# Kernel tuning notes

Hardware: AMD Instinct MI355X
Metric: run time of the kernel (lower is better)

## Reference

```python
import jax, jax.numpy as jnp
import numpy as np

VOCAB = 4194304
EMBED = 128
BATCH = 16384
NUM_DENSE = 13
NUM_CAT = 26
BOT_DIMS = (512, 256, 128)
TOP_DIMS = (1024, 1024, 512, 256, 1)


def _dense_params(key, fan_in, fan_out):
    kw, kb = jax.random.split(key)
    w = jax.random.normal(kw, (fan_in, fan_out), jnp.float32) * np.sqrt(2.0 / (fan_in + fan_out))
    b = jax.random.normal(kb, (fan_out,), jnp.float32) * np.sqrt(1.0 / fan_out)
    return w, b


def setup_inputs() -> dict:
    key = jax.random.key(0)
    ks = jax.random.split(key, 16)
    inp = {}
    inp['x_dense'] = jax.random.normal(ks[0], (BATCH, NUM_DENSE), jnp.float32)
    inp['x_cat'] = jax.random.randint(ks[1], (BATCH, NUM_CAT), 0, VOCAB, dtype=jnp.int32)
    # embedding table: uniform(0,1) * 1/sqrt(vocab)
    inp['embedding_table'] = jax.random.uniform(ks[2], (VOCAB, EMBED), jnp.float32) * np.float32(1.0 / np.sqrt(VOCAB))
    # bottom MLP params
    fan_in = NUM_DENSE
    for i, d in enumerate(BOT_DIMS):
        w, b = _dense_params(ks[3 + i], fan_in, d)
        inp[f'w_bot{i}'], inp[f'b_bot{i}'] = w, b
        fan_in = d
    # top MLP params; input dim = embed_dim + n_triu(27) = 128 + 378 = 506
    n_feat = 1 + NUM_CAT  # 27
    fan_in = EMBED + n_feat * (n_feat + 1) // 2
    for i, d in enumerate(TOP_DIMS):
        w, b = _dense_params(ks[8 + i], fan_in, d)
        inp[f'w_top{i}'], inp[f'b_top{i}'] = w, b
        fan_in = d
    return inp


def _forward(x_dense, x_cat, embedding_table,
             w_bot0, b_bot0, w_bot1, b_bot1, w_bot2, b_bot2,
             w_top0, b_top0, w_top1, b_top1, w_top2, b_top2,
             w_top3, b_top3, w_top4, b_top4):
    B = x_dense.shape[0]
    # bottom MLP
    h = x_dense
    for w, b in ((w_bot0, b_bot0), (w_bot1, b_bot1), (w_bot2, b_bot2)):
        h = jax.nn.relu(h @ w + b)
    bot_out = h  # [B, 128]
    feat = bot_out.reshape(B, -1, EMBED)  # [B, 1, 128]
    # embedding gather (irregular access)
    idx = (x_cat.reshape(-1) % VOCAB)
    emb = embedding_table[idx].reshape(B, NUM_CAT, EMBED)  # [B, 26, 128]
    stack = jnp.concatenate([feat, emb], axis=1)  # [B, 27, 128]
    # self interaction + upper-triangular (incl. diagonal) extraction
    xact = jnp.einsum('bnd,bmd->bnm', stack, stack)  # [B, 27, 27]
    i, j = jnp.triu_indices(stack.shape[1])
    inter = xact[:, i, j]  # [B, 378]
    top = jnp.concatenate([bot_out, inter], axis=-1)  # [B, 506]
    tops = ((w_top0, b_top0), (w_top1, b_top1), (w_top2, b_top2), (w_top3, b_top3), (w_top4, b_top4))
    for li, (w, b) in enumerate(tops):
        top = top @ w + b
        if li < len(tops) - 1:
            top = jax.nn.relu(top)
    return top  # [B, 1] logits


def reference(x_dense, x_cat, embedding_table,
              w_bot0, b_bot0, w_bot1, b_bot1, w_bot2, b_bot2,
              w_top0, b_top0, w_top1, b_top1, w_top2, b_top2,
              w_top3, b_top3, w_top4, b_top4):
    return _forward(x_dense, x_cat, embedding_table,
                    w_bot0, b_bot0, w_bot1, b_bot1, w_bot2, b_bot2,
                    w_top0, b_top0, w_top1, b_top1, w_top2, b_top2,
                    w_top3, b_top3, w_top4, b_top4)
```

## Files before the change

kernel.cpp:

```cpp
#include <hip/hip_runtime.h>
#include <cstdint>
#include <cstddef>

#define BATCH 16384
#define VOCAB_MASK (4194304 - 1)

typedef __attribute__((ext_vector_type(4))) float f32x4;
typedef __attribute__((ext_vector_type(8))) __bf16 bf16x8;
typedef __attribute__((ext_vector_type(4))) __bf16 bf16x4;

static_assert(sizeof(bf16x8) == 16, "bf16x8 must be 16 bytes");

static __device__ __forceinline__ __bf16 f2bf(float f) {
  union { float f; unsigned u; } in; in.f = f;
  unsigned r = in.u + 0x7FFF + ((in.u >> 16) & 1);
  union { unsigned short s; __bf16 b; } out; out.s = (unsigned short)(r >> 16);
  return out.b;
}
static __device__ __forceinline__ float bf2f(__bf16 b) {
  union { __bf16 b; unsigned short s; } in; in.b = b;
  union { unsigned u; float f; } out; out.u = ((unsigned)in.s) << 16;
  return out.f;
}

#define GLDS16(g, l) __builtin_amdgcn_global_load_lds( \
    (const __attribute__((address_space(1))) unsigned int*)(g), \
    (__attribute__((address_space(3))) unsigned int*)(l), 16, 0, 0)

static __device__ __forceinline__ unsigned swz16(unsigned b) {
  return b ^ ((((b >> 6) & 3u) ^ ((b >> 8) & 3u)) << 4);
}
static __device__ __forceinline__ bf16x8 lds_frag(const char* smem, unsigned base,
                                                  unsigned r, unsigned cg) {
  unsigned b = r * 64u + cg;
  return *(const bf16x8*)(smem + base + swz16(b));
}

struct TJob { const float* W; __bf16* WT; int K, N, Kp, tx, off; };
struct TJobs { TJob j[7]; };

__global__ __launch_bounds__(256) void transpose_all(TJobs js, int njobs)
{
  __shared__ float tile[64][65];
  int b = blockIdx.x;
  int ji = 0;
  #pragma unroll
  for (int i = 1; i < 7; ++i) if (i < njobs && b >= js.j[i].off) ji = i;
  const TJob jb = js.j[ji];
  int lb = b - jb.off;
  int bx = lb % jb.tx, by = lb / jb.tx;
  const int kb = bx * 64, nb = by * 64;
  const int tx = threadIdx.x & 63, ty = threadIdx.x >> 6;
  #pragma unroll
  for (int i = 0; i < 64; i += 4) {
    int k = kb + ty + i, n = nb + tx;
    tile[ty + i][tx] = (k < jb.K && n < jb.N) ? jb.W[(size_t)k * jb.N + n] : 0.f;
  }
  __syncthreads();
  #pragma unroll
  for (int i = 0; i < 64; i += 4) {
    int n = nb + ty + i, k = kb + tx;
    if (n < jb.N && k < jb.Kp) jb.WT[(size_t)n * jb.Kp + k] = f2bf(tile[tx][ty + i]);
  }
}

__global__ __launch_bounds__(256) void bottom_fused(
    const float* __restrict__ x,
    const __bf16* __restrict__ w0t, const float* __restrict__ b0,
    const __bf16* __restrict__ w1t, const float* __restrict__ b1,
    const __bf16* __restrict__ w2t, const float* __restrict__ b2,
    __bf16* __restrict__ h2out)
{
  __shared__ __bf16 h0s[32][520];
  __shared__ __bf16 h1s[32][264];
  __shared__ __bf16 As[32][40];
  __shared__ __bf16 Bs[256][32];
  const int tid = threadIdx.x, lane = tid & 63, w = tid >> 6;
  const int r0 = blockIdx.x * 32;
  const int srow_b = lane >> 2;
  const int scol_b = (lane & 3) * 8;
  const unsigned rA = lane & 15, cgw = (lane >> 4) * 8;

  for (int idx = tid; idx < 32 * 40; idx += 256) {
    int row = idx / 40, k = idx - row * 40;
    float v = (k < 13) ? x[(size_t)(r0 + row) * 13 + k] : 0.f;
    As[row][k] = f2bf(v);
  }

  #pragma unroll
  for (int p = 0; p < 2; ++p) {
    __syncthreads();
    #pragma unroll
    for (int c = 0; c < 4; ++c) {
      int row = w * 64 + c * 16 + srow_b;
      GLDS16(w0t + (size_t)(p * 256 + row) * 32 + scol_b, &Bs[row][scol_b]);
    }
    __syncthreads();
    bf16x8 a[2], bv[4];
    #pragma unroll
    for (int m = 0; m < 2; ++m) a[m] = *(const bf16x8*)&As[rA + m * 16][cgw];
    #pragma unroll
    for (int n = 0; n < 4; ++n) bv[n] = *(const bf16x8*)&Bs[w * 64 + n * 16 + rA][cgw];
    f32x4 acc[2][4] = {};
    #pragma unroll
    for (int m = 0; m < 2; ++m)
      #pragma unroll
      for (int n = 0; n < 4; ++n)
        acc[m][n] = __builtin_amdgcn_mfma_f32_16x16x32_bf16(a[m], bv[n], acc[m][n], 0, 0, 0);
    #pragma unroll
    for (int m = 0; m < 2; ++m)
      #pragma unroll
      for (int n = 0; n < 4; ++n) {
        int col = p * 256 + w * 64 + n * 16 + (int)rA;
        float bb = b0[col];
        #pragma unroll
        for (int r = 0; r < 4; ++r) {
          int row = m * 16 + (lane >> 4) * 4 + r;
          h0s[row][col] = f2bf(fmaxf(acc[m][n][r] + bb, 0.f));
        }
      }
  }

  f32x4 acc1[2][4] = {};
  for (int k0 = 0; k0 < 512; k0 += 32) {
    __syncthreads();
    #pragma unroll
    for (int c = 0; c < 4; ++c) {
      int row = w * 64 + c * 16 + srow_b;
      GLDS16(w1t + (size_t)row * 512 + k0 + scol_b, &Bs[row][scol_b]);
    }
    __syncthreads();
    bf16x8 a[2], bv[4];
    #pragma unroll
    for (int m = 0; m < 2; ++m) a[m] = *(const bf16x8*)&h0s[rA + m * 16][k0 + cgw];
    #pragma unroll
    for (int n = 0; n < 4; ++n) bv[n] = *(const bf16x8*)&Bs[w * 64 + n * 16 + rA][cgw];
    #pragma unroll
    for (int m = 0; m < 2; ++m)
      #pragma unroll
      for (int n = 0; n < 4; ++n)
        acc1[m][n] = __builtin_amdgcn_mfma_f32_16x16x32_bf16(a[m], bv[n], acc1[m][n], 0, 0, 0);
  }
  #pragma unroll
  for (int m = 0; m < 2; ++m)
    #pragma unroll
    for (int n = 0; n < 4; ++n) {
      int col = w * 64 + n * 16 + (int)rA;
      float bb = b1[col];
      #pragma unroll
      for (int r = 0; r < 4; ++r) {
        int row = m * 16 + (lane >> 4) * 4 + r;
        h1s[row][col] = f2bf(fmaxf(acc1[m][n][r] + bb, 0.f));
      }
    }

  f32x4 acc2[2][2] = {};
  for (int k0 = 0; k0 < 256; k0 += 32) {
    __syncthreads();
    #pragma unroll
    for (int c = 0; c < 2; ++c) {
      int row = w * 32 + c * 16 + srow_b;
      GLDS16(w2t + (size_t)row * 256 + k0 + scol_b, &Bs[row][scol_b]);
    }
    __syncthreads();
    bf16x8 a[2], bv[2];
    #pragma unroll
    for (int m = 0; m < 2; ++m) a[m] = *(const bf16x8*)&h1s[rA + m * 16][k0 + cgw];
    #pragma unroll
    for (int n = 0; n < 2; ++n) bv[n] = *(const bf16x8*)&Bs[w * 32 + n * 16 + rA][cgw];
    #pragma unroll
    for (int m = 0; m < 2; ++m)
      #pragma unroll
      for (int n = 0; n < 2; ++n)
        acc2[m][n] = __builtin_amdgcn_mfma_f32_16x16x32_bf16(a[m], bv[n], acc2[m][n], 0, 0, 0);
  }
  #pragma unroll
  for (int m = 0; m < 2; ++m)
    #pragma unroll
    for (int n = 0; n < 2; ++n) {
      int col = w * 32 + n * 16 + (int)rA;
      float bb = b2[col];
      #pragma unroll
      for (int r = 0; r < 4; ++r) {
        int row = m * 16 + (lane >> 4) * 4 + r;
        h2out[(size_t)(r0 + row) * 128 + col] = f2bf(fmaxf(acc2[m][n][r] + bb, 0.f));
      }
    }
}

__global__ __launch_bounds__(256) void interact_mfma(
    const __bf16* __restrict__ bot, const int* __restrict__ xcat,
    const float* __restrict__ emb, __bf16* __restrict__ top_in)
{
  __shared__ __bf16 st[4][32][136];
  const int tid = threadIdx.x, lane = tid & 63, w = tid >> 6;
  const int s = blockIdx.x * 4 + w;

  const int* xr = xcat + (size_t)s * 26;
  float4 buf[13];
  #pragma unroll
  for (int i = 0; i < 13; ++i) {
    int fi = 2 * i + (lane >> 5);
    int ridx = xr[fi] & VOCAB_MASK;
    buf[i] = *(const float4*)(emb + (size_t)ridx * 128 + (lane & 31) * 4);
  }

  *(unsigned*)&st[w][0][lane * 2] = *(const unsigned*)(bot + (size_t)s * 128 + lane * 2);
  #pragma unroll
  for (int r = 27; r < 32; ++r) *(unsigned*)&st[w][r][lane * 2] = 0u;
  #pragma unroll
  for (int i = 0; i < 13; ++i) {
    int row = 1 + 2 * i + (lane >> 5);
    bf16x4 bv;
    bv[0] = f2bf(buf[i].x); bv[1] = f2bf(buf[i].y);
    bv[2] = f2bf(buf[i].z); bv[3] = f2bf(buf[i].w);
    *(bf16x4*)&st[w][row][(lane & 31) * 4] = bv;
  }

  f32x4 a00 = {}, a01 = {}, a11 = {};
  #pragma unroll
  for (int k0 = 0; k0 < 4; ++k0) {
    bf16x8 fr0 = *(const bf16x8*)&st[w][(lane & 15)][k0 * 32 + (lane >> 4) * 8];
    bf16x8 fr1 = *(const bf16x8*)&st[w][16 + (lane & 15)][k0 * 32 + (lane >> 4) * 8];
    a00 = __builtin_amdgcn_mfma_f32_16x16x32_bf16(fr0, fr0, a00, 0, 0, 0);
    a01 = __builtin_amdgcn_mfma_f32_16x16x32_bf16(fr0, fr1, a01, 0, 0, 0);
    a11 = __builtin_amdgcn_mfma_f32_16x16x32_bf16(fr1, fr1, a11, 0, 0, 0);
  }

  __bf16* op = top_in + (size_t)s * 512;
  ((unsigned*)op)[lane] = *(const unsigned*)&st[w][0][lane * 2];
  if (lane < 3) ((unsigned*)op)[253 + lane] = 0u;

  const int jc = lane & 15, rb = (lane >> 4) * 4;
  #pragma unroll
  for (int r = 0; r < 4; ++r) {
    {
      int i = rb + r, j = jc;
      if (i <= j) op[128 + i * 27 - i * (i - 1) / 2 + (j - i)] = f2bf(a00[r]);
    }
    {
      int i = rb + r, j = 16 + jc;
      if (j <= 26) op[128 + i * 27 - i * (i - 1) / 2 + (j - i)] = f2bf(a01[r]);
    }
    {
      int i = 16 + rb + r, j = 16 + jc;
      if (i <= j && j <= 26) op[128 + i * 27 - i * (i - 1) / 2 + (j - i)] = f2bf(a11[r]);
    }
  }
}

__global__ __launch_bounds__(512, 4) void gemm_8ph_bm128(
    const __bf16* __restrict__ A, const __bf16* __restrict__ WT,
    const float* __restrict__ bias, __bf16* __restrict__ C,
    int N, int sA, int K, int gm)
{
  __shared__ __align__(16) char smem[49152];
  const int tid = threadIdx.x, lane = tid & 63, w = tid >> 6;
  const int wm = w >> 2, wn = w & 3;

  int nb = gridDim.x;
  int id = blockIdx.x;
  int swz = ((nb & 7) == 0) ? ((id & 7) * (nb >> 3) + (id >> 3)) : id;
  const int m0 = (swz % gm) * 128, n0 = (swz / gm) * 256;

  unsigned LdA; const __bf16* sApA;
  {
    unsigned L = (unsigned)w * 1024u + (unsigned)lane * 16u;
    unsigned Ls = swz16(L);
    LdA = L;
    sApA = A + (size_t)(m0 + (Ls >> 6)) * sA + ((Ls & 63) >> 1);
  }
  unsigned LdB[2]; const __bf16* sBp[2];
  #pragma unroll
  for (int h = 0; h < 2; ++h) {
    unsigned L = h * 8192u + (unsigned)w * 1024u + (unsigned)lane * 16u;
    unsigned Ls = swz16(L);
    LdB[h] = L;
    sBp[h] = WT + (size_t)(n0 + (Ls >> 6)) * K + ((Ls & 63) >> 1);
  }

  #define STAGE_A1(kt, p) { GLDS16(sApA + (kt)*32, smem + (p)*24576 + LdA); }
  #define STAGE_B2(kt, p) { GLDS16(sBp[0] + (kt)*32, smem + (p)*24576 + 8192 + LdB[0]); \
                            GLDS16(sBp[1] + (kt)*32, smem + (p)*24576 + 8192 + LdB[1]); }

  const unsigned cg = (lane >> 4) * 16u;
  const unsigned rA = (lane & 15);

  f32x4 acc[4][4] = {};
  const int iters = (K >> 5) >> 1;

  STAGE_B2(0, 0); STAGE_A1(0, 0); STAGE_B2(1, 1);
  asm volatile("s_waitcnt vmcnt(2)" ::: "memory");
  __builtin_amdgcn_s_barrier();
  __builtin_amdgcn_sched_barrier(0);

  for (int i = 0; i < iters; ++i) {
    const int t = 2 * i;
    const bool more = (i + 1 < iters);

    bf16x8 a0[2], b0[4];
    #pragma unroll
    for (int m = 0; m < 2; ++m) a0[m] = lds_frag(smem, 0, wm * 64 + m * 16 + rA, cg);
    #pragma unroll
    for (int n = 0; n < 4; ++n) b0[n] = lds_frag(smem, 8192, wn * 64 + n * 16 + rA, cg);
    STAGE_A1(t + 1, 1);
    __builtin_amdgcn_s_barrier();
    asm volatile("s_waitcnt lgkmcnt(0)" ::: "memory");
    __builtin_amdgcn_sched_barrier(0);
    __builtin_amdgcn_s_setprio(1);
    #pragma unroll
    for (int m = 0; m < 2; ++m)
      #pragma unroll
      for (int n = 0; n < 4; ++n)
        acc[m][n] = __builtin_amdgcn_mfma_f32_16x16x32_bf16(a0[m], b0[n], acc[m][n], 0, 0, 0);
    __builtin_amdgcn_s_setprio(0);
    __builtin_amdgcn_s_barrier();
    __builtin_amdgcn_sched_barrier(0);

    bf16x8 a1[2];
    #pragma unroll
    for (int m = 0; m < 2; ++m) a1[m] = lds_frag(smem, 0, wm * 64 + 32 + m * 16 + rA, cg);
    if (more) STAGE_B2(t + 2, 0);
    __builtin_amdgcn_s_barrier();
    asm volatile("s_waitcnt lgkmcnt(0)" ::: "memory");
    __builtin_amdgcn_sched_barrier(0);
    __builtin_amdgcn_s_setprio(1);
    #pragma unroll
    for (int m = 0; m < 2; ++m)
      #pragma unroll
      for (int n = 0; n < 4; ++n)
        acc[2 + m][n] = __builtin_amdgcn_mfma_f32_16x16x32_bf16(a1[m], b0[n], acc[2 + m][n], 0, 0, 0);
    __builtin_amdgcn_s_setprio(0);
    if (more) { asm volatile("s_waitcnt vmcnt(2)" ::: "memory"); }
    else      { asm volatile("s_waitcnt vmcnt(0)" ::: "memory"); }
    __builtin_amdgcn_s_barrier();
    __builtin_amdgcn_sched_barrier(0);

    bf16x8 a2[2], b2[4];
    #pragma unroll
    for (int m = 0; m < 2; ++m) a2[m] = lds_frag(smem, 24576, wm * 64 + m * 16 + rA, cg);
    #pragma unroll
    for (int n = 0; n < 4; ++n) b2[n] = lds_frag(smem, 24576 + 8192, wn * 64 + n * 16 + rA, cg);
    if (more) STAGE_A1(t + 2, 0);
    __builtin_amdgcn_s_barrier();
    asm volatile("s_waitcnt lgkmcnt(0)" ::: "memory");
    __builtin_amdgcn_sched_barrier(0);
    __builtin_amdgcn_s_setprio(1);
    #pragma unroll
    for (int m = 0; m < 2; ++m)
      #pragma unroll
      for (int n = 0; n < 4; ++n)
        acc[m][n] = __builtin_amdgcn_mfma_f32_16x16x32_bf16(a2[m], b2[n], acc[m][n], 0, 0, 0);
    __builtin_amdgcn_s_setprio(0);
    __builtin_amdgcn_s_barrier();
    __builtin_amdgcn_sched_barrier(0);

    bf16x8 a3[2];
    #pragma unroll
    for (int m = 0; m < 2; ++m) a3[m] = lds_frag(smem, 24576, wm * 64 + 32 + m * 16 + rA, cg);
    if (more) STAGE_B2(t + 3, 1);
    __builtin_amdgcn_s_barrier();
    asm volatile("s_waitcnt lgkmcnt(0)" ::: "memory");
    __builtin_amdgcn_sched_barrier(0);
    __builtin_amdgcn_s_setprio(1);
    #pragma unroll
    for (int m = 0; m < 2; ++m)
      #pragma unroll
      for (int n = 0; n < 4; ++n)
        acc[2 + m][n] = __builtin_amdgcn_mfma_f32_16x16x32_bf16(a3[m], b2[n], acc[2 + m][n], 0, 0, 0);
    __builtin_amdgcn_s_setprio(0);
    if (more) { asm volatile("s_waitcnt vmcnt(2)" ::: "memory"); }
    __builtin_amdgcn_s_barrier();
    __builtin_amdgcn_sched_barrier(0);
  }

  #pragma unroll
  for (int n = 0; n < 4; ++n) {
    int col = n0 + wn * 64 + n * 16 + (lane & 15);
    float bv = bias[col];
    #pragma unroll
    for (int m = 0; m < 4; ++m) {
      #pragma unroll
      for (int r = 0; r < 4; ++r) {
        int row = m0 + wm * 64 + m * 16 + (lane >> 4) * 4 + r;
        float v = fmaxf(acc[m][n][r] + bv, 0.f);
        C[(size_t)row * N + col] = f2bf(v);
      }
    }
  }
  #undef STAGE_A1
  #undef STAGE_B2
}

__global__ __launch_bounds__(512, 2) void gemm_8ph_n128(
    const __bf16* __restrict__ A, const __bf16* __restrict__ WT,
    const float* __restrict__ bias, __bf16* __restrict__ C,
    int N, int sA, int K, int gm)
{
  __shared__ __align__(16) char smem[49152];
  const int tid = threadIdx.x, lane = tid & 63, w = tid >> 6;
  const int wm = w >> 1, wn = w & 1;

  int nb = gridDim.x;
  int id = blockIdx.x;
  int swz = ((nb & 7) == 0) ? ((id & 7) * (nb >> 3) + (id >> 3)) : id;
  const int m0 = (swz % gm) * 256, n0 = (swz / gm) * 128;

  unsigned Ld[2]; const __bf16* sAp[2]; const __bf16* sBp0;
  #pragma unroll
  for (int h = 0; h < 2; ++h) {
    unsigned L = h * 8192u + (unsigned)w * 1024u + (unsigned)lane * 16u;
    unsigned Ls = swz16(L);
    Ld[h] = L;
    int srow = Ls >> 6, scb = Ls & 63;
    sAp[h] = A + (size_t)(m0 + srow) * sA + (scb >> 1);
  }
  {
    unsigned L = (unsigned)w * 1024u + (unsigned)lane * 16u;
    unsigned Ls = swz16(L);
    int srow = Ls >> 6, scb = Ls & 63;
    sBp0 = WT + (size_t)(n0 + srow) * K + (scb >> 1);
  }

  #define STAGE_A2(kt, p) { GLDS16(sAp[0] + (kt)*32, smem + (p)*24576 + Ld[0]); \
                            GLDS16(sAp[1] + (kt)*32, smem + (p)*24576 + Ld[1]); }
  #define STAGE_B1(kt, p) { GLDS16(sBp0 + (kt)*32, smem + (p)*24576 + 16384 + Ld[0]); }

  const unsigned cg = (lane >> 4) * 16u;
  const unsigned rA = (lane & 15);

  f32x4 acc[4][4] = {};
  const int iters = (K >> 5) >> 1;

  STAGE_B1(0, 0); STAGE_A2(0, 0); STAGE_B1(1, 1);
  asm volatile("s_waitcnt vmcnt(1)" ::: "memory");
  __builtin_amdgcn_s_barrier();
  __builtin_amdgcn_sched_barrier(0);

  for (int i = 0; i < iters; ++i) {
    const int t = 2 * i;
    const bool more = (i + 1 < iters);

    bf16x8 a0[2], b0[4];
    #pragma unroll
    for (int m = 0; m < 2; ++m) a0[m] = lds_frag(smem, 0, wm * 64 + m * 16 + rA, cg);
    #pragma unroll
    for (int n = 0; n < 4; ++n) b0[n] = lds_frag(smem, 16384, wn * 64 + n * 16 + rA, cg);
    STAGE_A2(t + 1, 1);
    __builtin_amdgcn_s_barrier();
    asm volatile("s_waitcnt lgkmcnt(0)" ::: "memory");
    __builtin_amdgcn_sched_barrier(0);
    __builtin_amdgcn_s_setprio(1);
    #pragma unroll
    for (int m = 0; m < 2; ++m)
      #pragma unroll
      for (int n = 0; n < 4; ++n)
        acc[m][n] = __builtin_amdgcn_mfma_f32_16x16x32_bf16(a0[m], b0[n], acc[m][n], 0, 0, 0);
    __builtin_amdgcn_s_setprio(0);
    __builtin_amdgcn_s_barrier();
    __builtin_amdgcn_sched_barrier(0);

    bf16x8 a1[2];
    #pragma unroll
    for (int m = 0; m < 2; ++m) a1[m] = lds_frag(smem, 0, wm * 64 + 32 + m * 16 + rA, cg);
    if (more) STAGE_B1(t + 2, 0);
    __builtin_amdgcn_s_barrier();
    asm volatile("s_waitcnt lgkmcnt(0)" ::: "memory");
    __builtin_amdgcn_sched_barrier(0);
    __builtin_amdgcn_s_setprio(1);
    #pragma unroll
    for (int m = 0; m < 2; ++m)
      #pragma unroll
      for (int n = 0; n < 4; ++n)
        acc[2 + m][n] = __builtin_amdgcn_mfma_f32_16x16x32_bf16(a1[m], b0[n], acc[2 + m][n], 0, 0, 0);
    __builtin_amdgcn_s_setprio(0);
    if (more) { asm volatile("s_waitcnt vmcnt(1)" ::: "memory"); }
    else      { asm volatile("s_waitcnt vmcnt(0)" ::: "memory"); }
    __builtin_amdgcn_s_barrier();
    __builtin_amdgcn_sched_barrier(0);

    bf16x8 a2[2], b2[4];
    #pragma unroll
    for (int m = 0; m < 2; ++m) a2[m] = lds_frag(smem, 24576, wm * 64 + m * 16 + rA, cg);
    #pragma unroll
    for (int n = 0; n < 4; ++n) b2[n] = lds_frag(smem, 24576 + 16384, wn * 64 + n * 16 + rA, cg);
    if (more) STAGE_A2(t + 2, 0);
    __builtin_amdgcn_s_barrier();
    asm volatile("s_waitcnt lgkmcnt(0)" ::: "memory");
    __builtin_amdgcn_sched_barrier(0);
    __builtin_amdgcn_s_setprio(1);
    #pragma unroll
    for (int m = 0; m < 2; ++m)
      #pragma unroll
      for (int n = 0; n < 4; ++n)
        acc[m][n] = __builtin_amdgcn_mfma_f32_16x16x32_bf16(a2[m], b2[n], acc[m][n], 0, 0, 0);
    __builtin_amdgcn_s_setprio(0);
    __builtin_amdgcn_s_barrier();
    __builtin_amdgcn_sched_barrier(0);

    bf16x8 a3[2];
    #pragma unroll
    for (int m = 0; m < 2; ++m) a3[m] = lds_frag(smem, 24576, wm * 64 + 32 + m * 16 + rA, cg);
    if (more) STAGE_B1(t + 3, 1);
    __builtin_amdgcn_s_barrier();
    asm volatile("s_waitcnt lgkmcnt(0)" ::: "memory");
    __builtin_amdgcn_sched_barrier(0);
    __builtin_amdgcn_s_setprio(1);
    #pragma unroll
    for (int m = 0; m < 2; ++m)
      #pragma unroll
      for (int n = 0; n < 4; ++n)
        acc[2 + m][n] = __builtin_amdgcn_mfma_f32_16x16x32_bf16(a3[m], b2[n], acc[2 + m][n], 0, 0, 0);
    __builtin_amdgcn_s_setprio(0);
    if (more) { asm volatile("s_waitcnt vmcnt(1)" ::: "memory"); }
    __builtin_amdgcn_s_barrier();
    __builtin_amdgcn_sched_barrier(0);
  }

  #pragma unroll
  for (int n = 0; n < 4; ++n) {
    int col = n0 + wn * 64 + n * 16 + (lane & 15);
    float bv = bias[col];
    #pragma unroll
    for (int m = 0; m < 4; ++m) {
      #pragma unroll
      for (int r = 0; r < 4; ++r) {
        int row = m0 + wm * 64 + m * 16 + (lane >> 4) * 4 + r;
        float v = fmaxf(acc[m][n][r] + bv, 0.f);
        C[(size_t)row * N + col] = f2bf(v);
      }
    }
  }
  #undef STAGE_A2
  #undef STAGE_B1
}

__global__ __launch_bounds__(256) void gemm_t3_final(
    const __bf16* __restrict__ A, const __bf16* __restrict__ WT,
    const float* __restrict__ b3, const float* __restrict__ w4,
    const float* __restrict__ b4, float* __restrict__ out)
{
  __shared__ __bf16 As[128][32];
  __shared__ __bf16 Bs[256][32];
  __shared__ float red[128][4];
  const int tid = threadIdx.x, lane = tid & 63, wid = tid >> 6;
  const int m0 = blockIdx.x * 128;
  const int srow = wid * 16 + (lane >> 2);
  const int scol = (lane & 3) * 8;
  const __bf16* Ag0 = A + (size_t)(m0 + srow) * 512 + scol;
  const __bf16* Ag1 = A + (size_t)(m0 + srow + 64) * 512 + scol;

  f32x4 acc[8][4] = {};

  for (int k0 = 0; k0 < 512; k0 += 32) {
    __syncthreads();
    GLDS16(Ag0 + k0, &As[srow][scol]);
    GLDS16(Ag1 + k0, &As[srow + 64][scol]);
    #pragma unroll
    for (int c = 0; c < 4; ++c) {
      int br = wid * 64 + c * 16 + (lane >> 2);
      GLDS16(WT + (size_t)br * 512 + k0 + scol, &Bs[br][scol]);
    }
    __syncthreads();

    bf16x8 af[8], bfv[4];
    #pragma unroll
    for (int m = 0; m < 8; ++m)
      af[m] = *(const bf16x8*)&As[m * 16 + (lane & 15)][(lane >> 4) * 8];
    #pragma unroll
    for (int n = 0; n < 4; ++n)
      bfv[n] = *(const bf16x8*)&Bs[wid * 64 + n * 16 + (lane & 15)][(lane >> 4) * 8];
    #pragma unroll
    for (int m = 0; m < 8; ++m)
      #pragma unroll
      for (int n = 0; n < 4; ++n)
        acc[m][n] = __builtin_amdgcn_mfma_f32_16x16x32_bf16(af[m], bfv[n], acc[m][n], 0, 0, 0);
  }

  float pd[8][4];
  #pragma unroll
  for (int m = 0; m < 8; ++m)
    #pragma unroll
    for (int r = 0; r < 4; ++r) pd[m][r] = 0.f;
  #pragma unroll
  for (int n = 0; n < 4; ++n) {
    int col = wid * 64 + n * 16 + (lane & 15);
    float bb = b3[col];
    float wc = w4[col];
    #pragma unroll
    for (int m = 0; m < 8; ++m)
      #pragma unroll
      for (int r = 0; r < 4; ++r)
        pd[m][r] += fmaxf(acc[m][n][r] + bb, 0.f) * wc;
  }
  #pragma unroll
  for (int m = 0; m < 8; ++m)
    #pragma unroll
    for (int r = 0; r < 4; ++r) {
      float s = pd[m][r];
      s += __shfl_xor(s, 1); s += __shfl_xor(s, 2);
      s += __shfl_xor(s, 4); s += __shfl_xor(s, 8);
      if ((lane & 15) == 0) red[m * 16 + (lane >> 4) * 4 + r][wid] = s;
    }
  __syncthreads();
  if (tid < 128)
    out[m0 + tid] = red[tid][0] + red[tid][1] + red[tid][2] + red[tid][3] + b4[0];
}

extern "C" void kernel_launch(void* const* d_in, const int* in_sizes, int n_in,
                              void* d_out, int out_size, void* d_ws, size_t ws_size,
                              hipStream_t stream)
{
  const float* x_dense = (const float*)d_in[0];
  const int*   x_cat   = (const int*)d_in[1];
  const float* emb     = (const float*)d_in[2];
  const float* wb[3] = {(const float*)d_in[3], (const float*)d_in[5], (const float*)d_in[7]};
  const float* bb[3] = {(const float*)d_in[4], (const float*)d_in[6], (const float*)d_in[8]};
  const float* wt[5] = {(const float*)d_in[9],  (const float*)d_in[11], (const float*)d_in[13],
                        (const float*)d_in[15], (const float*)d_in[17]};
  const float* bt[5] = {(const float*)d_in[10], (const float*)d_in[12], (const float*)d_in[14],
                        (const float*)d_in[16], (const float*)d_in[18]};
  float* out = (float*)d_out;

  char* ws = (char*)d_ws;
  const size_t MB = 1ull << 20;
  __bf16* wt_b0 = (__bf16*)(ws + 0 * MB);
  __bf16* wt_b1 = (__bf16*)(ws + 1 * MB);
  __bf16* wt_b2 = (__bf16*)(ws + 2 * MB);
  __bf16* wt_t0 = (__bf16*)(ws + 3 * MB);
  __bf16* wt_t1 = (__bf16*)(ws + 4 * MB);
  __bf16* wt_t2 = (__bf16*)(ws + 6 * MB);
  __bf16* wt_t3 = (__bf16*)(ws + 7 * MB);
  __bf16* h2     = (__bf16*)(ws + 8 * MB);
  __bf16* top_in = (__bf16*)(ws + 12 * MB);
  __bf16* t2     = (__bf16*)(ws + 12 * MB);
  __bf16* t1     = (__bf16*)(ws + 28 * MB);
  __bf16* t0     = (__bf16*)(ws + 60 * MB);

  TJobs js;
  const float* Ws[7] = {wb[0], wb[1], wb[2], wt[0], wt[1], wt[2], wt[3]};
  __bf16* WTs[7] = {wt_b0, wt_b1, wt_b2, wt_t0, wt_t1, wt_t2, wt_t3};
  int Ks[7]  = {13, 512, 256, 506, 1024, 1024, 512};
  int Ns[7]  = {512, 256, 128, 1024, 1024, 512, 256};
  int Kps[7] = {32, 512, 256, 512, 1024, 1024, 512};
  int off = 0;
  for (int i = 0; i < 7; ++i) {
    int tx = (Kps[i] + 63) / 64, ty = (Ns[i] + 63) / 64;
    js.j[i] = TJob{Ws[i], WTs[i], Ks[i], Ns[i], Kps[i], tx, off};
    off += tx * ty;
  }
  transpose_all<<<dim3(off), dim3(256), 0, stream>>>(js, 7);

  bottom_fused<<<dim3(BATCH / 32), dim3(256), 0, stream>>>(
      x_dense, wt_b0, bb[0], wt_b1, bb[1], wt_b2, bb[2], h2);

  interact_mfma<<<dim3(BATCH / 4), dim3(256), 0, stream>>>(h2, x_cat, emb, top_in);

  gemm_8ph_bm128<<<dim3(512), dim3(512), 0, stream>>>(top_in, wt_t0, bt[0], t0, 1024, 512, 512, 128);
  gemm_8ph_bm128<<<dim3(512), dim3(512), 0, stream>>>(t0, wt_t1, bt[1], t1, 1024, 1024, 1024, 128);
  gemm_8ph_n128<<<dim3(256), dim3(512), 0, stream>>>(t1, wt_t2, bt[2], t2, 512, 1024, 1024, 64);

  gemm_t3_final<<<dim3(128), dim3(256), 0, stream>>>(t2, wt_t3, bt[3], wt[4], bt[4], out);
}
```

Measured before the change: 189.2 us.

## Replace top-MLP GEMM with 256x256 tile, 4-stage LDS pipeline kernel

Swaps the 128x256-tile double-buffered GEMM for the first two top-MLP layers for a 256x256-tile kernel with a 4-deep LDS ring (128 KB shared) and three k-tiles of prefetch in flight. The larger tile doubles per-wave accumulators and raises MFMA work per LDS fragment load. The deeper pipeline aims to hide global-load latency better. In exchange, grid size halves to 256 blocks, occupancy drops with the large LDS and register footprint, and the wait counts must match the deeper prefetch.

Result: slower. 202.5 us (+7.0%).

```diff
diff --git a/kernel.cpp b/kernel.cpp
--- a/kernel.cpp
+++ b/kernel.cpp
@@ -249,147 +249,118 @@
   }
 }
 
-__global__ __launch_bounds__(512, 4) void gemm_8ph_bm128(
+__global__ __launch_bounds__(512, 2) void gemm_deep(
     const __bf16* __restrict__ A, const __bf16* __restrict__ WT,
     const float* __restrict__ bias, __bf16* __restrict__ C,
     int N, int sA, int K, int gm)
 {
-  __shared__ __align__(16) char smem[49152];
+  __shared__ __align__(16) char smem[131072];
   const int tid = threadIdx.x, lane = tid & 63, w = tid >> 6;
   const int wm = w >> 2, wn = w & 3;
 
   int nb = gridDim.x;
   int id = blockIdx.x;
   int swz = ((nb & 7) == 0) ? ((id & 7) * (nb >> 3) + (id >> 3)) : id;
-  const int m0 = (swz % gm) * 128, n0 = (swz / gm) * 256;
-
-  unsigned LdA; const __bf16* sApA;
-  {
-    unsigned L = (unsigned)w * 1024u + (unsigned)lane * 16u;
-    unsigned Ls = swz16(L);
-    LdA = L;
-    sApA = A + (size_t)(m0 + (Ls >> 6)) * sA + ((Ls & 63) >> 1);
-  }
-  unsigned LdB[2]; const __bf16* sBp[2];
+  const int m0 = (swz % gm) * 256, n0 = (swz / gm) * 256;
+
+  unsigned Ld[2]; const __bf16* sAp[2]; const __bf16* sBp[2];
   #pragma unroll
   for (int h = 0; h < 2; ++h) {
     unsigned L = h * 8192u + (unsigned)w * 1024u + (unsigned)lane * 16u;
     unsigned Ls = swz16(L);
-    LdB[h] = L;
-    sBp[h] = WT + (size_t)(n0 + (Ls >> 6)) * K + ((Ls & 63) >> 1);
-  }
-
-  #define STAGE_A1(kt, p) { GLDS16(sApA + (kt)*32, smem + (p)*24576 + LdA); }
-  #define STAGE_B2(kt, p) { GLDS16(sBp[0] + (kt)*32, smem + (p)*24576 + 8192 + LdB[0]); \
-                            GLDS16(sBp[1] + (kt)*32, smem + (p)*24576 + 8192 + LdB[1]); }
+    Ld[h] = L;
+    int srow = Ls >> 6, scb = Ls & 63;
+    sAp[h] = A  + (size_t)(m0 + srow) * sA + (scb >> 1);
+    sBp[h] = WT + (size_t)(n0 + srow) * K  + (scb >> 1);
+  }
+
+  #define STAGE_A(kt, p) { GLDS16(sAp[0] + (size_t)(kt)*32, smem + (p)*32768 + Ld[0]); \
+                           GLDS16(sAp[1] + (size_t)(kt)*32, smem + (p)*32768 + Ld[1]); }
+  #define STAGE_B(kt, p) { GLDS16(sBp[0] + (size_t)(kt)*32, smem + (p)*32768 + 16384 + Ld[0]); \
+                           GLDS16(sBp[1] + (size_t)(kt)*32, smem + (p)*32768 + 16384 + Ld[1]); }
 
   const unsigned cg = (lane >> 4) * 16u;
   const unsigned rA = (lane & 15);
 
-  f32x4 acc[4][4] = {};
-  const int iters = (K >> 5) >> 1;
-
-  STAGE_B2(0, 0); STAGE_A1(0, 0); STAGE_B2(1, 1);
-  asm volatile("s_waitcnt vmcnt(2)" ::: "memory");
+  f32x4 acc[8][4] = {};
+  const int KT = K >> 5;
+
+  STAGE_B(0, 0); STAGE_A(0, 0);
+  STAGE_B(1, 1); STAGE_A(1, 1);
+  STAGE_B(2, 2); STAGE_A(2, 2);
+  asm volatile("s_waitcnt vmcnt(8)" ::: "memory");
   __builtin_amdgcn_s_barrier();
   __builtin_amdgcn_sched_barrier(0);
 
-  for (int i = 0; i < iters; ++i) {
-    const int t = 2 * i;
-    const bool more = (i + 1 < iters);
-
-    bf16x8 a0[2], b0[4];
-    #pragma unroll
-    for (int m = 0; m < 2; ++m) a0[m] = lds_frag(smem, 0, wm * 64 + m * 16 + rA, cg);
-    #pragma unroll
-    for (int n = 0; n < 4; ++n) b0[n] = lds_frag(smem, 8192, wn * 64 + n * 16 + rA, cg);
-    STAGE_A1(t + 1, 1);
-    __builtin_amdgcn_s_barrier();
-    asm volatile("s_waitcnt lgkmcnt(0)" ::: "memory");
-    __builtin_amdgcn_sched_barrier(0);
-    __builtin_amdgcn_s_setprio(1);
-    #pragma unroll
-    for (int m = 0; m < 2; ++m)
-      #pragma unroll
-      for (int n = 0; n < 4; ++n)
-        acc[m][n] = __builtin_amdgcn_mfma_f32_16x16x32_bf16(a0[m], b0[n], acc[m][n], 0, 0, 0);
-    __builtin_amdgcn_s_setprio(0);
-    __builtin_amdgcn_s_barrier();
-    __builtin_amdgcn_sched_barrier(0);
-
-    bf16x8 a1[2];
-    #pragma unroll
-    for (int m = 0; m < 2; ++m) a1[m] = lds_frag(smem, 0, wm * 64 + 32 + m * 16 + rA, cg);
-    if (more) STAGE_B2(t + 2, 0);
-    __builtin_amdgcn_s_barrier();
-    asm volatile("s_waitcnt lgkmcnt(0)" ::: "memory");
-    __builtin_amdgcn_sched_barrier(0);
-    __builtin_amdgcn_s_setprio(1);
-    #pragma unroll
-    for (int m = 0; m < 2; ++m)
-      #pragma unroll
-      for (int n = 0; n < 4; ++n)
-        acc[2 + m][n] = __builtin_amdgcn_mfma_f32_16x16x32_bf16(a1[m], b0[n], acc[2 + m][n], 0, 0, 0);
-    __builtin_amdgcn_s_setprio(0);
-    if (more) { asm volatile("s_waitcnt vmcnt(2)" ::: "memory"); }
-    else      { asm volatile("s_waitcnt vmcnt(0)" ::: "memory"); }
-    __builtin_amdgcn_s_barrier();
-    __builtin_amdgcn_sched_barrier(0);
-
-    bf16x8 a2[2], b2[4];
-    #pragma unroll
-    for (int m = 0; m < 2; ++m) a2[m] = lds_frag(smem, 24576, wm * 64 + m * 16 + rA, cg);
-    #pragma unroll
-    for (int n = 0; n < 4; ++n) b2[n] = lds_frag(smem, 24576 + 8192, wn * 64 + n * 16 + rA, cg);
-    if (more) STAGE_A1(t + 2, 0);
-    __builtin_amdgcn_s_barrier();
-    asm volatile("s_waitcnt lgkmcnt(0)" ::: "memory");
-    __builtin_amdgcn_sched_barrier(0);
-    __builtin_amdgcn_s_setprio(1);
-    #pragma unroll
-    for (int m = 0; m < 2; ++m)
-      #pragma unroll
-      for (int n = 0; n < 4; ++n)
-        acc[m][n] = __builtin_amdgcn_mfma_f32_16x16x32_bf16(a2[m], b2[n], acc[m][n], 0, 0, 0);
-    __builtin_amdgcn_s_setprio(0);
-    __builtin_amdgcn_s_barrier();
-    __builtin_amdgcn_sched_barrier(0);
-
-    bf16x8 a3[2];
-    #pragma unroll
-    for (int m = 0; m < 2; ++m) a3[m] = lds_frag(smem, 24576, wm * 64 + 32 + m * 16 + rA, cg);
-    if (more) STAGE_B2(t + 3, 1);
-    __builtin_amdgcn_s_barrier();
-    asm volatile("s_waitcnt lgkmcnt(0)" ::: "memory");
-    __builtin_amdgcn_sched_barrier(0);
-    __builtin_amdgcn_s_setprio(1);
-    #pragma unroll
-    for (int m = 0; m < 2; ++m)
-      #pragma unroll
-      for (int n = 0; n < 4; ++n)
-        acc[2 + m][n] = __builtin_amdgcn_mfma_f32_16x16x32_bf16(a3[m], b2[n], acc[2 + m][n], 0, 0, 0);
-    __builtin_amdgcn_s_setprio(0);
-    if (more) { asm volatile("s_waitcnt vmcnt(2)" ::: "memory"); }
-    __builtin_amdgcn_s_barrier();
-    __builtin_amdgcn_sched_barrier(0);
-  }
+  #define TILE_BODY(j) { \
+    const int t = mi * 4 + (j); \
+    const bool stg = (t + 3 < KT); \
+     \
+    bf16x8 a0[4], b0[4]; \
+    _Pragma("unroll") \
+    for (int m = 0; m < 4; ++m) a0[m] = lds_frag(smem, (j)*32768u, wm * 128 + m * 16 + rA, cg); \
+    _Pragma("unroll") \
+    for (int n = 0; n < 4; ++n) b0[n] = lds_frag(smem, (j)*32768u + 16384u, wn * 64 + n * 16 + rA, cg); \
+    if (stg) STAGE_A(t + 3, ((j) + 3) & 3); \
+    __builtin_amdgcn_s_barrier(); \
+    asm volatile("s_waitcnt lgkmcnt(0)" ::: "memory"); \
+    __builtin_amdgcn_sched_barrier(0); \
+    __builtin_amdgcn_s_setprio(1); \
+    _Pragma("unroll") \
+    for (int m = 0; m < 4; ++m) \
+      _Pragma("unroll") \
+      for (int n = 0; n < 4; ++n) \
+        acc[m][n] = __builtin_amdgcn_mfma_f32_16x16x32_bf16(a0[m], b0[n], acc[m][n], 0, 0, 0); \
+    __builtin_amdgcn_s_setprio(0); \
+    __builtin_amdgcn_s_barrier(); \
+    __builtin_amdgcn_sched_barrier(0); \
+     \
+    bf16x8 a1[4]; \
+    _Pragma("unroll") \
+    for (int m = 0; m < 4; ++m) a1[m] = lds_frag(smem, (j)*32768u, wm * 128 + 64 + m * 16 + rA, cg); \
+    if (stg) STAGE_B(t + 3, ((j) + 3) & 3); \
+    __builtin_amdgcn_s_barrier(); \
+    asm volatile("s_waitcnt lgkmcnt(0)" ::: "memory"); \
+    __builtin_amdgcn_sched_barrier(0); \
+    __builtin_amdgcn_s_setprio(1); \
+    _Pragma("unroll") \
+    for (int m = 0; m < 4; ++m) \
+      _Pragma("unroll") \
+      for (int n = 0; n < 4; ++n) \
+        acc[4 + m][n] = __builtin_amdgcn_mfma_f32_16x16x32_bf16(a1[m], b0[n], acc[4 + m][n], 0, 0, 0); \
+    __builtin_amdgcn_s_setprio(0); \
+    if (t + 4 <= KT - 1)      { asm volatile("s_waitcnt vmcnt(8)" ::: "memory"); } \
+    else if (t + 3 == KT - 1) { asm volatile("s_waitcnt vmcnt(4)" ::: "memory"); } \
+    else                      { asm volatile("s_waitcnt vmcnt(0)" ::: "memory"); } \
+    __builtin_amdgcn_s_barrier(); \
+    __builtin_amdgcn_sched_barrier(0); \
+  }
+
+  const int MI = KT >> 2;
+  for (int mi = 0; mi < MI; ++mi) {
+    TILE_BODY(0)
+    TILE_BODY(1)
+    TILE_BODY(2)
+    TILE_BODY(3)
+  }
+  #undef TILE_BODY
+  #undef STAGE_A
+  #undef STAGE_B
 
   #pragma unroll
   for (int n = 0; n < 4; ++n) {
     int col = n0 + wn * 64 + n * 16 + (lane & 15);
     float bv = bias[col];
     #pragma unroll
-    for (int m = 0; m < 4; ++m) {
+    for (int m = 0; m < 8; ++m) {
       #pragma unroll
       for (int r = 0; r < 4; ++r) {
-        int row = m0 + wm * 64 + m * 16 + (lane >> 4) * 4 + r;
+        int row = m0 + wm * 128 + m * 16 + (lane >> 4) * 4 + r;
         float v = fmaxf(acc[m][n][r] + bv, 0.f);
         C[(size_t)row * N + col] = f2bf(v);
       }
     }
   }
-  #undef STAGE_A1
-  #undef STAGE_B2
 }
 
 __global__ __launch_bounds__(512, 2) void gemm_8ph_n128(
@@ -656,8 +627,8 @@
 
   interact_mfma<<<dim3(BATCH / 4), dim3(256), 0, stream>>>(h2, x_cat, emb, top_in);
 
-  gemm_8ph_bm128<<<dim3(512), dim3(512), 0, stream>>>(top_in, wt_t0, bt[0], t0, 1024, 512, 512, 128);
-  gemm_8ph_bm128<<<dim3(512), dim3(512), 0, stream>>>(t0, wt_t1, bt[1], t1, 1024, 1024, 1024, 128);
+  gemm_deep<<<dim3(256), dim3(512), 0, stream>>>(top_in, wt_t0, bt[0], t0, 1024, 512, 512, 64);
+  gemm_deep<<<dim3(256), dim3(512), 0, stream>>>(t0, wt_t1, bt[1], t1, 1024, 1024, 1024, 64);
   gemm_8ph_n128<<<dim3(256), dim3(512), 0, stream>>>(t1, wt_t2, bt[2], t2, 512, 1024, 1024, 64);
 
   gemm_t3_final<<<dim3(128), dim3(256), 0, stream>>>(t2, wt_t3, bt[3], wt[4], bt[4], out);
```
